# Performance work log

Hardware: AMD Instinct MI355X
Metric: run time of the kernel (lower is better)

## Reference

```python
import jax, jax.numpy as jnp
import numpy as np

B, T, D = 4, 4096, 2048
E, C = 8, 512
O = 2048
I = D // E  # expert_in_features = 256


def setup_inputs() -> dict:
    key = jax.random.key(0)
    k1, k2, k3, k4, k5 = jax.random.split(key, 5)
    x = jax.random.normal(k1, (B, T, D), dtype=jnp.float32)
    combine_array = jax.random.uniform(k2, (B, T, E, C), dtype=jnp.float32)
    dispatch_mask = jax.random.uniform(k3, (B, T, E, C), dtype=jnp.float32)
    weight = jax.random.normal(k4, (E, O, I), dtype=jnp.float32) * (1.0 / np.sqrt(I))
    bias = jax.random.normal(k5, (O,), dtype=jnp.float32) * 0.01
    return {"x": x, "combine_array": combine_array, "dispatch_mask": dispatch_mask,
            "weight": weight, "bias": bias}


def reference(x, combine_array, dispatch_mask, weight, bias):
    b, t, d = x.shape
    e, o, i = weight.shape
    # dispatch: one-hot gather of tokens into expert capacity slots
    xr = x.reshape(b, t, e, i)                                   # [B,T,E,I]
    xd = jnp.einsum('btei,btec->beci', xr, dispatch_mask)        # [B,E,C,I]
    # bias homogenization trick: append 1 to features, bias column to weight
    x_homo = jnp.concatenate([xd, jnp.ones_like(xd[..., :1])], axis=-1)       # [B,E,C,I+1]
    b_col = jnp.broadcast_to(bias.reshape(1, o, 1), (e, o, 1))
    w_homo = jnp.concatenate([weight, b_col], axis=-1)                        # [E,O,I+1]
    # per-expert linear then combine scatter back to tokens
    y = jnp.einsum('beci,eoi->beco', x_homo, w_homo)             # [B,E,C,O]
    out = jnp.einsum('beco,btec->bto', y, combine_array)         # [B,T,O]
    return out
```

## Files before the change

kernel.cpp:

```cpp
#include <hip/hip_runtime.h>

typedef float f32x4 __attribute__((ext_vector_type(4)));
typedef short s16x8 __attribute__((ext_vector_type(8)));
typedef short s16x4 __attribute__((ext_vector_type(4)));
typedef unsigned u32x4 __attribute__((ext_vector_type(4)));
typedef unsigned u32x2 __attribute__((ext_vector_type(2)));

#define DEVI __device__ __forceinline__

static constexpr int B_ = 4, T_ = 4096, D_ = 2048, E_ = 8, C_ = 512, O_ = 2048, I_ = 256;
static constexpr size_t XDN = (size_t)B_ * E_ * I_ * C_;

DEVI short f2bf(float f) {
  unsigned u = __builtin_bit_cast(unsigned, f);
  u += 0x7FFFu + ((u >> 16) & 1u);
  return (short)(u >> 16);
}

DEVI unsigned cvtpk(float lo, float hi) {
  unsigned r;
  asm("v_cvt_pk_bf16_f32 %0, %1, %2" : "=v"(r) : "v"(lo), "v"(hi));
  return r;
}

DEVI void gll16(const short* gsrc, short* ldst) {
  __builtin_amdgcn_global_load_lds(
      (const __attribute__((address_space(1))) void*)gsrc,
      (__attribute__((address_space(3))) void*)ldst, 16, 0, 0);
}

__global__ __launch_bounds__(512, 2) void k_gemm1(const float* __restrict__ x,
                                                  const float* __restrict__ disp,
                                                  const float* __restrict__ w,
                                                  short* __restrict__ wT,
                                                  float* __restrict__ xdP) {
  __shared__ short lXT[128 * 64];
  __shared__ short lDT[256 * 64];
  const int tid = threadIdx.x;
  const int bid = blockIdx.x;

  if (bid >= 256) {
    const int pb = bid - 256;
#pragma unroll
    for (int u = 0; u < 2; u++) {
      const int idx = (pb * 512 + tid) * 2 + u;
      const int o = idx >> 9;
      const int dd = (idx & 511) << 2;
      const int e = dd >> 8, i = dd & 255;
      f32x4 v = *(const f32x4*)(w + (((size_t)e * O_ + o) * I_ + i));
      u32x2 p = {cvtpk(v[0], v[1]), cvtpk(v[2], v[3])};
      const int dsw = (dd & ~63) | (dd & 7) | ((((dd >> 3) & 7) ^ (o & 7)) << 3);
      *(u32x2*)(wT + (size_t)o * D_ + dsw) = p;
    }
    return;
  }

  const int xcd = bid & 7, slot = bid >> 3;
  const int grp = (slot >> 2) * 8 + xcd;
  const int jj = slot & 3;
  const int be = grp >> 1, kc = grp & 1;
  const int mt = jj >> 1, nt = jj & 1;
  const int b = be >> 3, e = be & 7;
  const int lane = tid & 63, wid = tid >> 6;
  const int wm = wid >> 2, wn = wid & 3;
  const int g = lane >> 4, lr = lane & 15;

  const size_t xbase = (size_t)b * T_ * D_ + (size_t)e * I_ + (size_t)mt * 128;
  const size_t dbase = (size_t)b * T_ * (E_ * C_) + (size_t)e * C_ + (size_t)nt * 256;

  const f32x4 z4 = {0.f, 0.f, 0.f, 0.f};
  f32x4 acc[4][4];
#pragma unroll
  for (int i = 0; i < 4; i++)
#pragma unroll
    for (int j = 0; j < 4; j++) acc[i][j] = z4;

  const int xt0 = (tid >> 4) * 2;
  const int xi8 = (tid & 15) * 8;
  const int dt0 = (tid >> 5) * 2;
  const int dc8 = (tid & 31) * 8;
  const int q7 = tid & 7;

  f32x4 xa0, xa1, xb0, xb1;
  f32x4 da[2][4];
  auto loadRegs = [&](int kt) {
    const float* sx = x + xbase + (size_t)(kt + xt0) * D_ + xi8;
    xa0 = *(const f32x4*)sx;
    xa1 = *(const f32x4*)(sx + 4);
    xb0 = *(const f32x4*)(sx + D_);
    xb1 = *(const f32x4*)(sx + D_ + 4);
#pragma unroll
    for (int tt = 0; tt < 2; tt++) {
      const float* sd = disp + dbase + (size_t)(kt + tt * 32 + dt0) * (E_ * C_) + dc8;
      da[tt][0] = *(const f32x4*)sd;
      da[tt][1] = *(const f32x4*)(sd + 4);
      da[tt][2] = *(const f32x4*)(sd + E_ * C_);
      da[tt][3] = *(const f32x4*)(sd + E_ * C_ + 4);
    }
  };
  auto writeLds = [&]() {
#pragma unroll
    for (int j = 0; j < 8; j++) {
      const int i = xi8 + j;
      const int ad = i * 64 + (xt0 ^ ((j ^ q7) << 3));
      float va = (j < 4) ? xa0[j] : xa1[j - 4];
      float vb = (j < 4) ? xb0[j] : xb1[j - 4];
      *(unsigned*)&lXT[ad] = cvtpk(va, vb);
    }
#pragma unroll
    for (int tt = 0; tt < 2; tt++)
#pragma unroll
      for (int j = 0; j < 8; j++) {
        const int c = dc8 + j;
        const int ad = c * 64 + ((tt * 32 + dt0) ^ ((j ^ q7) << 3));
        float ua = (j < 4) ? da[tt][0][j] : da[tt][1][j - 4];
        float ub = (j < 4) ? da[tt][2][j] : da[tt][3][j - 4];
        *(unsigned*)&lDT[ad] = cvtpk(ua, ub);
      }
  };

  const int k0 = kc * 2048, kend = k0 + 2048;
  loadRegs(k0);
  for (int kt = k0; kt < kend; kt += 64) {
    __syncthreads();
    writeLds();
    if (kt + 64 < kend) loadRegs(kt + 64);
    __syncthreads();
#pragma unroll
    for (int kk = 0; kk < 2; kk++) {
      const int tb = kk * 32 + g * 8;
      s16x8 af[4], bfr[4];
#pragma unroll
      for (int mi = 0; mi < 4; mi++) {
        const int r = wm * 64 + mi * 16 + lr;
        const int sws = (((r & 7) ^ ((r >> 3) & 7)) << 3);
        af[mi] = *(const s16x8*)&lXT[r * 64 + (tb ^ sws)];
      }
#pragma unroll
      for (int ni = 0; ni < 4; ni++) {
        const int r = wn * 64 + ni * 16 + lr;
        const int sws = (((r & 7) ^ ((r >> 3) & 7)) << 3);
        bfr[ni] = *(const s16x8*)&lDT[r * 64 + (tb ^ sws)];
      }
#pragma unroll
      for (int mi = 0; mi < 4; mi++)
#pragma unroll
        for (int ni = 0; ni < 4; ni++)
          acc[mi][ni] = __builtin_amdgcn_mfma_f32_16x16x32_bf16(af[mi], bfr[ni], acc[mi][ni], 0, 0, 0);
    }
  }

  float* op = xdP + (size_t)kc * XDN + (size_t)be * I_ * C_;
#pragma unroll
  for (int mi = 0; mi < 4; mi++)
#pragma unroll
    for (int ni = 0; ni < 4; ni++)
#pragma unroll
      for (int r = 0; r < 4; r++) {
        const int ig = mt * 128 + wm * 64 + mi * 16 + g * 4 + r;
        const int cg = nt * 256 + wn * 64 + ni * 16 + lr;
        op[(size_t)ig * C_ + cg] = acc[mi][ni][r];
      }
}

__global__ __launch_bounds__(256) void k_cvt(const float* __restrict__ xdP,
                                             short* __restrict__ xdT) {
  size_t idx = (size_t)blockIdx.x * 256 + threadIdx.x;
  f32x4 a = *(const f32x4*)(xdP + idx * 4);
  f32x4 b = *(const f32x4*)(xdP + XDN + idx * 4);
#pragma unroll
  for (int j = 0; j < 4; j++) a[j] += b[j];
  u32x2 p = {cvtpk(a[0], a[1]), cvtpk(a[2], a[3])};
  *(u32x2*)(xdT + idx * 4) = p;
}

__global__ __launch_bounds__(512, 2) void k_zgemm(const float* __restrict__ comb,
                                                  const short* __restrict__ xdT,
                                                  short* __restrict__ z,
                                                  float* __restrict__ Se) {
  __shared__ short lA[128 * 64];
  __shared__ short lB[256 * 64];
  const int tid = threadIdx.x;
  const int bid = blockIdx.x;
  const int be = bid >> 5, mt = bid & 31;
  const int b = be >> 3, e = be & 7;
  const int lane = tid & 63, wid = tid >> 6;
  const int wm = wid >> 2, wn = wid & 3;
  const int g = lane >> 4, lr = lane & 15;

  const size_t abase = (size_t)b * T_ * (E_ * C_) + (size_t)(mt * 128) * (E_ * C_) + (size_t)e * C_;
  const short* Bsrc = xdT + (size_t)be * I_ * C_;

  float rs[2] = {0.f, 0.f};
  const f32x4 z4 = {0.f, 0.f, 0.f, 0.f};
  f32x4 acc[4][4];
#pragma unroll
  for (int i = 0; i < 4; i++)
#pragma unroll
    for (int j = 0; j < 4; j++) acc[i][j] = z4;

  for (int ct = 0; ct < C_; ct += 64) {
    __syncthreads();
#pragma unroll
    for (int cc = 0; cc < 2; cc++) {
      const int q = tid + 512 * cc;
      const int row = q >> 3;
      const int k8 = (q & 7) << 3;
      const int sw = (row & 7) << 3;
      const float* sa = comb + abase + (size_t)row * (E_ * C_) + ct + k8;
      f32x4 a0 = *(const f32x4*)sa;
      f32x4 a1 = *(const f32x4*)(sa + 4);
      rs[cc] += a0[0] + a0[1] + a0[2] + a0[3] + a1[0] + a1[1] + a1[2] + a1[3];
      u32x4 pw = {cvtpk(a0[0], a0[1]), cvtpk(a0[2], a0[3]),
                  cvtpk(a1[0], a1[1]), cvtpk(a1[2], a1[3])};
      *(u32x4*)&lA[row * 64 + (k8 ^ sw)] = pw;
    }
#pragma unroll
    for (int cc = 0; cc < 4; cc++) {
      const int q = tid + 512 * cc;
      const int row = q >> 3;
      const int k8 = (q & 7) << 3;
      const int sw = (row & 7) << 3;
      s16x8 pb = *(const s16x8*)(Bsrc + (size_t)row * C_ + ct + k8);
      *(s16x8*)&lB[row * 64 + (k8 ^ sw)] = pb;
    }
    __syncthreads();
#pragma unroll
    for (int kk = 0; kk < 2; kk++) {
      const int kb = kk * 32 + g * 8;
      s16x8 af[4], bf[4];
#pragma unroll
      for (int mi = 0; mi < 4; mi++) {
        const int r = wm * 64 + mi * 16 + lr;
        af[mi] = *(const s16x8*)&lA[r * 64 + (kb ^ ((r & 7) << 3))];
      }
#pragma unroll
      for (int ni = 0; ni < 4; ni++) {
        const int r = wn * 64 + ni * 16 + lr;
        bf[ni] = *(const s16x8*)&lB[r * 64 + (kb ^ ((r & 7) << 3))];
      }
#pragma unroll
      for (int mi = 0; mi < 4; mi++)
#pragma unroll
        for (int ni = 0; ni < 4; ni++)
          acc[mi][ni] = __builtin_amdgcn_mfma_f32_16x16x32_bf16(af[mi], bf[ni], acc[mi][ni], 0, 0, 0);
    }
  }
#pragma unroll
  for (int cc = 0; cc < 2; cc++) {
    float v = rs[cc];
    v += __shfl_xor(v, 1);
    v += __shfl_xor(v, 2);
    v += __shfl_xor(v, 4);
    if ((tid & 7) == 0)
      Se[((size_t)b * E_ + e) * T_ + mt * 128 + (tid >> 3) + 64 * cc] = v;
  }
#pragma unroll
  for (int mi = 0; mi < 4; mi++)
#pragma unroll
    for (int ni = 0; ni < 4; ni++)
#pragma unroll
      for (int r = 0; r < 4; r++) {
        const int tg = mt * 128 + wm * 64 + mi * 16 + g * 4 + r;
        const int ig = wn * 64 + ni * 16 + lr;
        const int d = e * I_ + ig;
        const int dsw = (d & ~63) | (d & 7) | ((((d >> 3) & 7) ^ (tg & 7)) << 3);
        z[((size_t)b * T_ + tg) * D_ + dsw] = f2bf(acc[mi][ni][r]);
      }
}

__global__ __launch_bounds__(512, 2) void k_outgemm(const short* __restrict__ z,
                                                    const short* __restrict__ wT,
                                                    const float* __restrict__ bias,
                                                    const float* __restrict__ Se,
                                                    float* __restrict__ out) {
  __shared__ short lA[2][256 * 64];
  __shared__ short lB[2][256 * 64];
  const int tid = threadIdx.x;
  const int lane = tid & 63, wid = tid >> 6;
  const int wm = wid >> 2, wn = wid & 3;
  const int g = lane >> 4, lr = lane & 15;

  const int bid = blockIdx.x;
  const int swz = (bid & 7) * 64 + (bid >> 3);
  const int mt = swz >> 3, nt = swz & 7;
  const int row0 = mt * 256;
  const int col0 = nt * 256;

  const int srow = (wid << 4) + (lane >> 3);
  const int scol = (lane & 7) << 3;
  const short* Abase = z + (size_t)(row0 + srow) * D_ + scol;
  const short* Bbase = wT + (size_t)(col0 + srow) * D_ + scol;

  const f32x4 zero4 = {0.f, 0.f, 0.f, 0.f};
  f32x4 acc[8][4];
#pragma unroll
  for (int i = 0; i < 8; i++)
#pragma unroll
    for (int j = 0; j < 4; j++) acc[i][j] = zero4;

  s16x8 af[8], bf0[4], bf1[4];
  const int swr = (lr & 7) << 3;

  auto stageA = [&](int sl, int h, int dt) {
    gll16(Abase + (size_t)(h * 128) * D_ + dt, &lA[sl][(h * 128 + wid * 16) * 64]);
    gll16(Abase + (size_t)(h * 128 + 8) * D_ + dt, &lA[sl][(h * 128 + wid * 16 + 8) * 64]);
  };
  auto stageB = [&](int sl, int h, int dt) {
    gll16(Bbase + (size_t)(h * 128) * D_ + dt, &lB[sl][(h * 128 + wid * 16) * 64]);
    gll16(Bbase + (size_t)(h * 128 + 8) * D_ + dt, &lB[sl][(h * 128 + wid * 16 + 8) * 64]);
  };
  auto readA = [&](int sl, int mh) {
#pragma unroll
    for (int mi = 0; mi < 4; mi++) {
      const int r = mh * 128 + wm * 64 + mi * 16 + lr;
#pragma unroll
      for (int ks = 0; ks < 2; ks++)
        af[mi * 2 + ks] = *(const s16x8*)&lA[sl][r * 64 + ((ks * 32 + g * 8) ^ swr)];
    }
  };
  auto readB = [&](int sl, int nh, s16x8* arr) {
#pragma unroll
    for (int ni = 0; ni < 2; ni++) {
      const int r = nh * 128 + wn * 32 + ni * 16 + lr;
#pragma unroll
      for (int ks = 0; ks < 2; ks++)
        arr[ni * 2 + ks] = *(const s16x8*)&lB[sl][r * 64 + ((ks * 32 + g * 8) ^ swr)];
    }
  };
  auto mmaq = [&](int mh, int nh, const s16x8* bb) {
    __builtin_amdgcn_s_setprio(1);
#pragma unroll
    for (int mi = 0; mi < 4; mi++)
#pragma unroll
      for (int ni = 0; ni < 2; ni++)
#pragma unroll
        for (int ks = 0; ks < 2; ks++)
          acc[mh * 4 + mi][nh * 2 + ni] = __builtin_amdgcn_mfma_f32_16x16x32_bf16(
              af[mi * 2 + ks], bb[ni * 2 + ks], acc[mh * 4 + mi][nh * 2 + ni], 0, 0, 0);
    __builtin_amdgcn_s_setprio(0);
  };

#define SCH __builtin_amdgcn_sched_barrier(0)
#define BAR do { SCH; asm volatile("s_barrier"); SCH; } while (0)
#define WV(N) do { asm volatile("s_waitcnt vmcnt(" #N ")"); SCH; } while (0)

  stageA(0, 0, 0); stageB(0, 0, 0); stageB(0, 1, 0); stageA(0, 1, 0);
  stageA(1, 0, 64); stageB(1, 0, 64); stageB(1, 1, 64);
  WV(6); BAR;

  for (int j = 0; j < 15; ++j) {
    const int d1 = (2 * j + 1) * 64, d2 = (2 * j + 2) * 64, d3 = (2 * j + 3) * 64;
    readA(0, 0); readB(0, 0, bf0); stageA(1, 1, d1);
    BAR; mmaq(0, 0, bf0); BAR;
    readB(0, 1, bf1); stageA(0, 0, d2);
    BAR; mmaq(0, 1, bf1); BAR;
    readA(0, 1); stageB(0, 0, d2);
    BAR; mmaq(1, 0, bf0); BAR;
    stageB(0, 1, d2); WV(6);
    BAR; mmaq(1, 1, bf1); BAR;
    readA(1, 0); readB(1, 0, bf0); stageA(0, 1, d2);
    BAR; mmaq(0, 0, bf0); BAR;
    readB(1, 1, bf1); stageA(1, 0, d3);
    BAR; mmaq(0, 1, bf1); BAR;
    readA(1, 1); stageB(1, 0, d3);
    BAR; mmaq(1, 0, bf0); BAR;
    stageB(1, 1, d3); WV(6);
    BAR; mmaq(1, 1, bf1); BAR;
  }
  {
    readA(0, 0); readB(0, 0, bf0); stageA(1, 1, 1984);
    BAR; mmaq(0, 0, bf0); BAR;
    readB(0, 1, bf1);
    BAR; mmaq(0, 1, bf1); BAR;
    readA(0, 1);
    BAR; mmaq(1, 0, bf0); BAR;
    WV(4);
    BAR; mmaq(1, 1, bf1); BAR;
    readA(1, 0); readB(1, 0, bf0); WV(2);
    BAR; mmaq(0, 0, bf0); BAR;
    readB(1, 1, bf1); WV(0);
    BAR; mmaq(0, 1, bf1); BAR;
    readA(1, 1);
    BAR; mmaq(1, 0, bf0); BAR;
    mmaq(1, 1, bf1);
  }
#undef SCH
#undef BAR
#undef WV

  __syncthreads();
  float* sS = (float*)lA;
  if (tid < 256) {
    const int bb = row0 >> 12, tt = (row0 & (T_ - 1)) + tid;
    float s = 0.f;
#pragma unroll
    for (int e = 0; e < E_; e++)
      s += Se[((size_t)(bb * E_ + e) << 12) + tt];
    sS[tid] = s;
  }
  __syncthreads();

  float bia[4];
#pragma unroll
  for (int nh = 0; nh < 2; nh++)
#pragma unroll
    for (int ni = 0; ni < 2; ni++)
      bia[nh * 2 + ni] = bias[col0 + nh * 128 + wn * 32 + ni * 16 + lr];
#pragma unroll
  for (int mh = 0; mh < 2; mh++)
#pragma unroll
    for (int mi = 0; mi < 4; mi++)
#pragma unroll
      for (int r = 0; r < 4; r++) {
        const int tg = row0 + mh * 128 + wm * 64 + mi * 16 + g * 4 + r;
        const float s = sS[tg - row0];
#pragma unroll
        for (int nh = 0; nh < 2; nh++)
#pragma unroll
          for (int ni = 0; ni < 2; ni++) {
            const int og = col0 + nh * 128 + wn * 32 + ni * 16 + lr;
            out[(size_t)tg * O_ + og] = acc[mh * 4 + mi][nh * 2 + ni][r] + bia[nh * 2 + ni] * s;
          }
      }
}

extern "C" void kernel_launch(void* const* d_in, const int* in_sizes, int n_in,
                              void* d_out, int out_size, void* d_ws, size_t ws_size,
                              hipStream_t stream) {
  const float* x    = (const float*)d_in[0];
  const float* comb = (const float*)d_in[1];
  const float* disp = (const float*)d_in[2];
  const float* w    = (const float*)d_in[3];
  const float* bias = (const float*)d_in[4];
  float* out = (float*)d_out;

  char* ws = (char*)d_ws;
  short* wT  = (short*)(ws);
  short* xdT = (short*)(ws + 8388608);
  short* z   = (short*)(ws + 16777216);
  float* xdP = (float*)(ws + 16777216);
  float* Se  = (float*)(ws + 83886080);

  k_gemm1<<<dim3(1280), dim3(512), 0, stream>>>(x, disp, w, wT, xdP);
  k_cvt<<<dim3(4096), dim3(256), 0, stream>>>(xdP, xdT);
  k_zgemm<<<dim3(1024), dim3(512), 0, stream>>>(comb, xdT, z, Se);
  k_outgemm<<<dim3(512), dim3(512), 0, stream>>>(z, wT, bias, Se, out);
}
```

Before: 341.2 us.

## Replace double-buffered interleaved GEMM pipeline with single-buffered synchronous K loop

The output GEMM's hand-scheduled, double-buffered LDS pipeline is removed. It had staggered global-to-LDS loads, explicit vmcnt waits and barriers around MFMA quarters. In its place is a simple loop: sync, stage the whole A/B tile, sync, then read and compute. This halves LDS usage and removes the many barriers and the complex schedule. The cost is that global-load latency is no longer overlapped with MFMA work, and correctness now relies on __syncthreads waiting for the async LDS loads to land.

Measured after the change: 368.3 us. 1.08x slower.

```diff
diff --git a/kernel.cpp b/kernel.cpp
--- a/kernel.cpp
+++ b/kernel.cpp
@@ -274,8 +274,8 @@
                                                     const float* __restrict__ bias,
                                                     const float* __restrict__ Se,
                                                     float* __restrict__ out) {
-  __shared__ short lA[2][256 * 64];
-  __shared__ short lB[2][256 * 64];
+  __shared__ short lA[256 * 64];
+  __shared__ short lB[256 * 64];
   const int tid = threadIdx.x;
   const int lane = tid & 63, wid = tid >> 6;
   const int wm = wid >> 2, wn = wid & 3;
@@ -302,30 +302,31 @@
   s16x8 af[8], bf0[4], bf1[4];
   const int swr = (lr & 7) << 3;
 
-  auto stageA = [&](int sl, int h, int dt) {
-    gll16(Abase + (size_t)(h * 128) * D_ + dt, &lA[sl][(h * 128 + wid * 16) * 64]);
-    gll16(Abase + (size_t)(h * 128 + 8) * D_ + dt, &lA[sl][(h * 128 + wid * 16 + 8) * 64]);
-  };
-  auto stageB = [&](int sl, int h, int dt) {
-    gll16(Bbase + (size_t)(h * 128) * D_ + dt, &lB[sl][(h * 128 + wid * 16) * 64]);
-    gll16(Bbase + (size_t)(h * 128 + 8) * D_ + dt, &lB[sl][(h * 128 + wid * 16 + 8) * 64]);
-  };
-  auto readA = [&](int sl, int mh) {
+  auto stage = [&](int dt) {
+#pragma unroll
+    for (int h = 0; h < 2; h++) {
+      gll16(Abase + (size_t)(h * 128) * D_ + dt, &lA[(h * 128 + wid * 16) * 64]);
+      gll16(Abase + (size_t)(h * 128 + 8) * D_ + dt, &lA[(h * 128 + wid * 16 + 8) * 64]);
+      gll16(Bbase + (size_t)(h * 128) * D_ + dt, &lB[(h * 128 + wid * 16) * 64]);
+      gll16(Bbase + (size_t)(h * 128 + 8) * D_ + dt, &lB[(h * 128 + wid * 16 + 8) * 64]);
+    }
+  };
+  auto readA = [&](int mh) {
 #pragma unroll
     for (int mi = 0; mi < 4; mi++) {
       const int r = mh * 128 + wm * 64 + mi * 16 + lr;
 #pragma unroll
       for (int ks = 0; ks < 2; ks++)
-        af[mi * 2 + ks] = *(const s16x8*)&lA[sl][r * 64 + ((ks * 32 + g * 8) ^ swr)];
-    }
-  };
-  auto readB = [&](int sl, int nh, s16x8* arr) {
+        af[mi * 2 + ks] = *(const s16x8*)&lA[r * 64 + ((ks * 32 + g * 8) ^ swr)];
+    }
+  };
+  auto readB = [&](int nh, s16x8* arr) {
 #pragma unroll
     for (int ni = 0; ni < 2; ni++) {
       const int r = nh * 128 + wn * 32 + ni * 16 + lr;
 #pragma unroll
       for (int ks = 0; ks < 2; ks++)
-        arr[ni * 2 + ks] = *(const s16x8*)&lB[sl][r * 64 + ((ks * 32 + g * 8) ^ swr)];
+        arr[ni * 2 + ks] = *(const s16x8*)&lB[r * 64 + ((ks * 32 + g * 8) ^ swr)];
     }
   };
   auto mmaq = [&](int mh, int nh, const s16x8* bb) {
@@ -341,53 +342,18 @@
     __builtin_amdgcn_s_setprio(0);
   };
 
-#define SCH __builtin_amdgcn_sched_barrier(0)
-#define BAR do { SCH; asm volatile("s_barrier"); SCH; } while (0)
-#define WV(N) do { asm volatile("s_waitcnt vmcnt(" #N ")"); SCH; } while (0)
-
-  stageA(0, 0, 0); stageB(0, 0, 0); stageB(0, 1, 0); stageA(0, 1, 0);
-  stageA(1, 0, 64); stageB(1, 0, 64); stageB(1, 1, 64);
-  WV(6); BAR;
-
-  for (int j = 0; j < 15; ++j) {
-    const int d1 = (2 * j + 1) * 64, d2 = (2 * j + 2) * 64, d3 = (2 * j + 3) * 64;
-    readA(0, 0); readB(0, 0, bf0); stageA(1, 1, d1);
-    BAR; mmaq(0, 0, bf0); BAR;
-    readB(0, 1, bf1); stageA(0, 0, d2);
-    BAR; mmaq(0, 1, bf1); BAR;
-    readA(0, 1); stageB(0, 0, d2);
-    BAR; mmaq(1, 0, bf0); BAR;
-    stageB(0, 1, d2); WV(6);
-    BAR; mmaq(1, 1, bf1); BAR;
-    readA(1, 0); readB(1, 0, bf0); stageA(0, 1, d2);
-    BAR; mmaq(0, 0, bf0); BAR;
-    readB(1, 1, bf1); stageA(1, 0, d3);
-    BAR; mmaq(0, 1, bf1); BAR;
-    readA(1, 1); stageB(1, 0, d3);
-    BAR; mmaq(1, 0, bf0); BAR;
-    stageB(1, 1, d3); WV(6);
-    BAR; mmaq(1, 1, bf1); BAR;
-  }
-  {
-    readA(0, 0); readB(0, 0, bf0); stageA(1, 1, 1984);
-    BAR; mmaq(0, 0, bf0); BAR;
-    readB(0, 1, bf1);
-    BAR; mmaq(0, 1, bf1); BAR;
-    readA(0, 1);
-    BAR; mmaq(1, 0, bf0); BAR;
-    WV(4);
-    BAR; mmaq(1, 1, bf1); BAR;
-    readA(1, 0); readB(1, 0, bf0); WV(2);
-    BAR; mmaq(0, 0, bf0); BAR;
-    readB(1, 1, bf1); WV(0);
-    BAR; mmaq(0, 1, bf1); BAR;
-    readA(1, 1);
-    BAR; mmaq(1, 0, bf0); BAR;
+  for (int t = 0; t < 32; ++t) {
+    __syncthreads();
+    stage(t * 64);
+    __syncthreads();
+    readA(0); readB(0, bf0);
+    mmaq(0, 0, bf0);
+    readB(1, bf1);
+    mmaq(0, 1, bf1);
+    readA(1);
+    mmaq(1, 0, bf0);
     mmaq(1, 1, bf1);
   }
-#undef SCH
-#undef BAR
-#undef WV
 
   __syncthreads();
   float* sS = (float*)lA;
```
